# Kernel optimization log

Hardware: AMD Instinct MI355X
Metric: run time of the kernel (lower is better)

The kernel has to match this reference:

```python
import jax, jax.numpy as jnp
import numpy as np

EMBED_DIM = 1024
NUM_HEADS = 16
HEAD_DIM = EMBED_DIM // NUM_HEADS


def setup_inputs() -> dict:
    key = jax.random.key(0)
    ks = jax.random.split(key, 9)
    B, T, D = 2, 4096, EMBED_DIM
    scale = 1.0 / np.sqrt(D)
    x = jax.random.normal(ks[0], (B, T, D), dtype=jnp.float32)
    # nn.Linear weights stored as (out, in); we use (in, out) layout via transpose-free init
    Wq = jax.random.uniform(ks[1], (D, D), dtype=jnp.float32, minval=-scale, maxval=scale)
    Wk = jax.random.uniform(ks[2], (D, D), dtype=jnp.float32, minval=-scale, maxval=scale)
    Wv = jax.random.uniform(ks[3], (D, D), dtype=jnp.float32, minval=-scale, maxval=scale)
    Wo = jax.random.uniform(ks[4], (D, D), dtype=jnp.float32, minval=-scale, maxval=scale)
    bq = jax.random.uniform(ks[5], (D,), dtype=jnp.float32, minval=-scale, maxval=scale)
    bk = jax.random.uniform(ks[6], (D,), dtype=jnp.float32, minval=-scale, maxval=scale)
    bv = jax.random.uniform(ks[7], (D,), dtype=jnp.float32, minval=-scale, maxval=scale)
    bo = jax.random.uniform(ks[8], (D,), dtype=jnp.float32, minval=-scale, maxval=scale)
    return {"x": x, "Wq": Wq, "bq": bq, "Wk": Wk, "bk": bk,
            "Wv": Wv, "bv": bv, "Wo": Wo, "bo": bo}


def reference(x, Wq, bq, Wk, bk, Wv, bv, Wo, bo):
    B, T, D = x.shape
    H, Hd = NUM_HEADS, HEAD_DIM
    q = x @ Wq + bq  # [B,T,D]
    k = x @ Wk + bk
    v = x @ Wv + bv
    # [B,T,D] -> [B,H,T,Hd]
    q = q.reshape(B, T, H, Hd).transpose(0, 2, 1, 3)
    k = k.reshape(B, T, H, Hd).transpose(0, 2, 1, 3)
    v = v.reshape(B, T, H, Hd).transpose(0, 2, 1, 3)
    att = jnp.einsum('bhqd,bhkd->bhqk', q, k) / jnp.sqrt(jnp.float32(Hd))
    causal = jnp.tril(jnp.ones((T, T), dtype=bool))  # True = keep
    att = jnp.where(causal, att, -jnp.inf)
    att = jax.nn.softmax(att, axis=-1)
    out = jnp.einsum('bhqk,bhkd->bhqd', att, v)  # [B,H,T,Hd]
    out = out.transpose(0, 2, 1, 3).reshape(B, T, D)
    return out @ Wo + bo
```

## Files before the change

kernel.cpp:

```cpp
#include <hip/hip_runtime.h>
#include <hip/hip_bf16.h>
#include <math.h>

typedef __bf16 bf16;
typedef __attribute__((ext_vector_type(8))) __bf16 bf16x8;
typedef __attribute__((ext_vector_type(4))) __bf16 bf16x4;
typedef __attribute__((ext_vector_type(4))) short short4v;
typedef __attribute__((ext_vector_type(4))) float f32x4;

#define MFMA16(a,b,c)  __builtin_amdgcn_mfma_f32_16x16x32_bf16((a),(b),(c),0,0,0)
#define MFMAK16(a,b,c) __builtin_amdgcn_mfma_f32_16x16x16bf16_1k((a),(b),(c),0,0,0)

__device__ __forceinline__ void gload16(const void* gp, void* lp) {
  __builtin_amdgcn_global_load_lds(
      (const __attribute__((address_space(1))) void*)gp,
      (__attribute__((address_space(3))) void*)lp, 16, 0, 0);
}

__global__ __launch_bounds__(256) void cast_x(
    const float* __restrict__ x, bf16* __restrict__ xb)
{
  size_t i = ((size_t)blockIdx.x*256 + threadIdx.x) * 8;
  f32x4 a = *(const f32x4*)(x+i);
  f32x4 b = *(const f32x4*)(x+i+4);
  bf16x8 o;
  #pragma unroll
  for (int j=0;j<4;j++) { o[j] = (bf16)a[j]; o[4+j] = (bf16)b[j]; }
  *(bf16x8*)(xb+i) = o;
}

__global__ __launch_bounds__(1024) void tr_cast(
    const float* __restrict__ w0, const float* __restrict__ w1,
    const float* __restrict__ w2, bf16* __restrict__ dst)
{
  __shared__ bf16 tile[64][65];
  const float* src = (blockIdx.z==0)?w0:(blockIdx.z==1)?w1:w2;
  bf16* d = dst + (size_t)blockIdx.z * (1024*1024);
  int x = threadIdx.x, y = threadIdx.y;
  int tc = blockIdx.x, tr = blockIdx.y;
  #pragma unroll
  for (int i=0;i<4;i++) {
    int r = y + i*16;
    tile[r][x] = (bf16)src[(size_t)(tr*64+r)*1024 + tc*64 + x];
  }
  __syncthreads();
  #pragma unroll
  for (int i=0;i<4;i++) {
    int r = y + i*16;
    d[(size_t)(tc*64+r)*1024 + tr*64 + x] = tile[x][r];
  }
}

__global__ __launch_bounds__(1024) void v_tr(
    const bf16* __restrict__ v, bf16* __restrict__ vt)
{
  __shared__ bf16 tile[64][65];
  int x = threadIdx.x, y = threadIdx.y;
  int tt = blockIdx.x;
  int bh = blockIdx.y;
  int b = bh >> 4, h = bh & 15;
  const bf16* src = v + ((size_t)b*4096 + tt*64)*1024 + h*64;
  bf16* dst = vt + ((size_t)bh*64)*4096 + tt*64;
  #pragma unroll
  for (int i=0;i<4;i++) {
    int r = y + i*16;
    tile[r][x] = src[(size_t)r*1024 + x];
  }
  __syncthreads();
  #pragma unroll
  for (int i=0;i<4;i++) {
    int r = y + i*16;
    dst[(size_t)r*4096 + x] = tile[x][r];
  }
}

__global__ __launch_bounds__(256) void gemm_qkv(
    const bf16* __restrict__ A, const bf16* __restrict__ Bt,
    const float* __restrict__ bq, const float* __restrict__ bk, const float* __restrict__ bv,
    bf16* __restrict__ q, bf16* __restrict__ k, bf16* __restrict__ v,
    int M, int K)
{
  __shared__ __align__(16) bf16 As[128*32];
  __shared__ __align__(16) bf16 Bs[128*32];
  const int tid  = threadIdx.x;
  const int wave = tid >> 6;
  const int lane = tid & 63;
  const int l15  = lane & 15;
  const int quad = lane >> 4;
  const int m0 = blockIdx.y * 128;
  const int n0 = blockIdx.x * 128;
  const int wm = (wave >> 1) * 64;
  const int wn = (wave & 1) * 64;
  const int srow = lane >> 2;
  const int scol = (lane & 3) * 8;

  f32x4 acc[4][4];
  #pragma unroll
  for (int i=0;i<4;i++)
    #pragma unroll
    for (int j=0;j<4;j++)
      acc[i][j] = (f32x4){0.f,0.f,0.f,0.f};

  for (int k0 = 0; k0 < K; k0 += 32) {
    __syncthreads();
    #pragma unroll
    for (int p=0;p<2;p++) {
      int c = p*4 + wave;
      int row = c*16 + srow;
      gload16(A  + (size_t)(m0+row)*K + k0 + scol, As + c*512);
      gload16(Bt + (size_t)(n0+row)*K + k0 + scol, Bs + c*512);
    }
    __syncthreads();
    bf16x8 af[4], bfr[4];
    #pragma unroll
    for (int t=0;t<4;t++) {
      af[t]  = *(const bf16x8*)(As + (wm + t*16 + l15)*32 + quad*8);
      bfr[t] = *(const bf16x8*)(Bs + (wn + t*16 + l15)*32 + quad*8);
    }
    #pragma unroll
    for (int mt=0;mt<4;mt++)
      #pragma unroll
      for (int nt=0;nt<4;nt++)
        acc[mt][nt] = MFMA16(af[mt], bfr[nt], acc[mt][nt]);
  }

  const int mat = n0 >> 10;
  const float* bsel = (mat==0) ? bq : (mat==1) ? bk : bv;
  bf16*       osel  = (mat==0) ? q  : (mat==1) ? k  : v;
  const float qsc   = (mat==0) ? 0.1803368801f : 1.0f;
  #pragma unroll
  for (int nt=0;nt<4;nt++) {
    int col = n0 + wn + nt*16 + l15;
    int cw  = col & 1023;
    float bvv = bsel[cw];
    #pragma unroll
    for (int mt=0;mt<4;mt++) {
      int row = m0 + wm + mt*16 + quad*4;
      #pragma unroll
      for (int r=0;r<4;r++)
        osel[(size_t)(row + r)*1024 + cw] = (bf16)((acc[mt][nt][r] + bvv) * qsc);
    }
  }
}

__global__ __launch_bounds__(256) void gemm_out(
    const bf16* __restrict__ A, const bf16* __restrict__ Bt,
    const float* __restrict__ bias, float* __restrict__ C,
    int M, int N, int K)
{
  __shared__ __align__(16) bf16 As[128*32];
  __shared__ __align__(16) bf16 Bs[128*32];
  const int tid  = threadIdx.x;
  const int wave = tid >> 6;
  const int lane = tid & 63;
  const int l15  = lane & 15;
  const int quad = lane >> 4;
  const int m0 = blockIdx.y * 128;
  const int n0 = blockIdx.x * 128;
  const int wm = (wave >> 1) * 64;
  const int wn = (wave & 1) * 64;
  const int srow = lane >> 2;
  const int scol = (lane & 3) * 8;

  f32x4 acc[4][4];
  #pragma unroll
  for (int i=0;i<4;i++)
    #pragma unroll
    for (int j=0;j<4;j++)
      acc[i][j] = (f32x4){0.f,0.f,0.f,0.f};

  for (int k0 = 0; k0 < K; k0 += 32) {
    __syncthreads();
    #pragma unroll
    for (int p=0;p<2;p++) {
      int c = p*4 + wave;
      int row = c*16 + srow;
      gload16(A  + (size_t)(m0+row)*K + k0 + scol, As + c*512);
      gload16(Bt + (size_t)(n0+row)*K + k0 + scol, Bs + c*512);
    }
    __syncthreads();
    bf16x8 af[4], bfr[4];
    #pragma unroll
    for (int t=0;t<4;t++) {
      af[t]  = *(const bf16x8*)(As + (wm + t*16 + l15)*32 + quad*8);
      bfr[t] = *(const bf16x8*)(Bs + (wn + t*16 + l15)*32 + quad*8);
    }
    #pragma unroll
    for (int mt=0;mt<4;mt++)
      #pragma unroll
      for (int nt=0;nt<4;nt++)
        acc[mt][nt] = MFMA16(af[mt], bfr[nt], acc[mt][nt]);
  }

  #pragma unroll
  for (int nt=0;nt<4;nt++) {
    int col = n0 + wn + nt*16 + l15;
    float bvv = bias[col];
    #pragma unroll
    for (int mt=0;mt<4;mt++) {
      int row = m0 + wm + mt*16 + quad*4;
      #pragma unroll
      for (int r=0;r<4;r++)
        C[(size_t)(row + r)*N + col] = acc[mt][nt][r] + bvv;
    }
  }
}

__global__ __launch_bounds__(256, 2) void attn_fwd(
    const bf16* __restrict__ Q, const bf16* __restrict__ Kp,
    const bf16* __restrict__ Vtg, bf16* __restrict__ O)
{
  __shared__ __align__(16) char KsB[2*8192];
  __shared__ __align__(16) char VtB[2*8192];

  const int tid  = threadIdx.x;
  const int w    = tid >> 6;
  const int lane = tid & 63;
  const int l15  = lane & 15;
  const int quad = lane >> 4;

  const int bid = blockIdx.x;
  const int pp  = bid >> 5;
  const int bh  = bid & 31;
  const int h   = bh & 15;
  const int b   = bh >> 4;

  const size_t headoff = (size_t)h * 64;
  const size_t bbase   = (size_t)b * 4096;

  short4v ones_s;
  {
    bf16x4 o1;
    #pragma unroll
    for (int j=0;j<4;j++) o1[j] = (bf16)1.0f;
    ones_s = __builtin_bit_cast(short4v, o1);
  }

  const int kt_row = tid >> 2;
  const int kswz   = (kt_row & 7) << 4;
  const int ks_w0  = kt_row*128 + (((tid & 3)*32)      ^ kswz);
  const int ks_w1  = kt_row*128 + (((tid & 3)*32 + 16) ^ kswz);

  const int vd  = tid >> 2;
  const int vt0 = (tid & 3) * 16;
  int vw[4];
  #pragma unroll
  for (int u=0;u<4;u++)
    vw[u] = vd*128 + (((vt0 + u*4)*2) ^ ((vd & 15) << 3));

  const int s7    = l15 & 7;
  const int ks_r0 = l15*128 + ((quad ^ (s7 & 3)) << 4) + ((s7 >> 2) << 6);
  const int ks_r1 = ks_r0 ^ 64;
  const int vt_rbase = l15*128 + ((quad ^ (l15 & 3)) << 3) + ((l15 >> 2) << 5);
  int vt_r[4];
  #pragma unroll
  for (int tt=0;tt<4;tt++) vt_r[tt] = vt_rbase ^ (tt << 5);

  const bf16* kbase0 = Kp  + (bbase + kt_row)*1024 + headoff + (tid & 3)*16;
  const bf16* vbase0 = Vtg + ((size_t)(bh*64) + vd)*4096 + vt0;

  for (int ph = 0; ph < 2; ++ph) {
    const int qt = ph ? (31 - pp) : pp;
    const int q0 = qt * 128;
    const int ktmax = 2*qt + 1;

    bf16x8 aqA[2], aqB[2];
    {
      int rowA = q0 + w*16 + l15;
      const bf16* qp = Q + (bbase + rowA)*1024 + headoff + quad*8;
      aqA[0] = *(const bf16x8*)(qp);
      aqA[1] = *(const bf16x8*)(qp + 32);
      qp += 64*1024;
      aqB[0] = *(const bf16x8*)(qp);
      aqB[1] = *(const bf16x8*)(qp + 32);
    }

    f32x4 accoA[4], accoB[4], accliA, accliB;
    #pragma unroll
    for (int i=0;i<4;i++) { accoA[i] = (f32x4){0.f,0.f,0.f,0.f}; accoB[i] = (f32x4){0.f,0.f,0.f,0.f}; }
    accliA = (f32x4){0.f,0.f,0.f,0.f};
    accliB = (f32x4){0.f,0.f,0.f,0.f};

    __syncthreads();
    {
      bf16x8 k0 = *(const bf16x8*)(kbase0);
      bf16x8 k1 = *(const bf16x8*)(kbase0 + 8);
      *(bf16x8*)(KsB + ks_w0) = k0;
      *(bf16x8*)(KsB + ks_w1) = k1;
      bf16x8 v0 = *(const bf16x8*)(vbase0);
      bf16x8 v1 = *(const bf16x8*)(vbase0 + 8);
      *(bf16x4*)(VtB + vw[0]) = __builtin_shufflevector(v0, v0, 0,1,2,3);
      *(bf16x4*)(VtB + vw[1]) = __builtin_shufflevector(v0, v0, 4,5,6,7);
      *(bf16x4*)(VtB + vw[2]) = __builtin_shufflevector(v1, v1, 0,1,2,3);
      *(bf16x4*)(VtB + vw[3]) = __builtin_shufflevector(v1, v1, 4,5,6,7);
    }
    __syncthreads();

    const bf16* kpref = kbase0 + 64*1024;
    const bf16* vpref = vbase0 + 64;

    for (int kt = 0; kt <= ktmax; ++kt) {
      const int p = kt & 1;
      const bool pre = (kt < ktmax);

      bf16x8 kr0, kr1, vr0, vr1;
      if (pre) {
        kr0 = *(const bf16x8*)(kpref);
        kr1 = *(const bf16x8*)(kpref + 8);
        vr0 = *(const bf16x8*)(vpref);
        vr1 = *(const bf16x8*)(vpref + 8);
        kpref += 64*1024;
        vpref += 64;
      }

      const char* ksb = KsB + p*8192;
      const char* vtb = VtB + p*8192;

      f32x4 accsA[4], accsB[4];
      #pragma unroll
      for (int i=0;i<4;i++) { accsA[i] = (f32x4){0.f,0.f,0.f,0.f}; accsB[i] = (f32x4){0.f,0.f,0.f,0.f}; }

      __builtin_amdgcn_s_setprio(1);
      #pragma unroll
      for (int kk=0;kk<2;kk++) {
        #pragma unroll
        for (int tt=0;tt<4;tt++) {
          bf16x8 ka = *(const bf16x8*)(ksb + (kk ? ks_r1 : ks_r0) + tt*2048);
          accsA[tt] = MFMA16(ka, aqA[kk], accsA[tt]);
          accsB[tt] = MFMA16(ka, aqB[kk], accsB[tt]);
        }
      }
      __builtin_amdgcn_s_setprio(0);

      short4v ptsA[4], ptsB[4];
      if (kt < 2*qt) {
        #pragma unroll
        for (int tt=0;tt<4;tt++) {
          bf16x4 pa, pb;
          #pragma unroll
          for (int r=0;r<4;r++) {
            pa[r] = (bf16)__builtin_amdgcn_exp2f(fminf(accsA[tt][r], 60.0f));
            pb[r] = (bf16)__builtin_amdgcn_exp2f(fminf(accsB[tt][r], 60.0f));
          }
          ptsA[tt] = __builtin_bit_cast(short4v, pa);
          ptsB[tt] = __builtin_bit_cast(short4v, pb);
        }
      } else {
        const bool adead = (kt > 2*qt);
        #pragma unroll
        for (int tt=0;tt<4;tt++) {
          bf16x4 pa, pb;
          #pragma unroll
          for (int r=0;r<4;r++) {
            const bool tq = (tt*16 + quad*4 + r > w*16 + l15);
            float fa = __builtin_amdgcn_exp2f(fminf(accsA[tt][r], 60.0f));
            if (adead || tq) fa = 0.0f;
            float fb = __builtin_amdgcn_exp2f(fminf(accsB[tt][r], 60.0f));
            if (adead && tq) fb = 0.0f;
            pa[r] = (bf16)fa; pb[r] = (bf16)fb;
          }
          ptsA[tt] = __builtin_bit_cast(short4v, pa);
          ptsB[tt] = __builtin_bit_cast(short4v, pb);
        }
      }

      __builtin_amdgcn_s_setprio(1);
      #pragma unroll
      for (int nt=0;nt<4;nt++) {
        #pragma unroll
        for (int tt=0;tt<4;tt++) {
          bf16x4 va = *(const bf16x4*)(vtb + vt_r[tt] + nt*2048);
          short4v vas = __builtin_bit_cast(short4v, va);
          accoA[nt] = MFMAK16(vas, ptsA[tt], accoA[nt]);
          accoB[nt] = MFMAK16(vas, ptsB[tt], accoB[nt]);
        }
      }
      #pragma unroll
      for (int tt=0;tt<4;tt++) {
        accliA = MFMAK16(ones_s, ptsA[tt], accliA);
        accliB = MFMAK16(ones_s, ptsB[tt], accliB);
      }
      __builtin_amdgcn_s_setprio(0);

      if (pre) {
        char* ksn = KsB + (p^1)*8192;
        char* vtn = VtB + (p^1)*8192;
        *(bf16x8*)(ksn + ks_w0) = kr0;
        *(bf16x8*)(ksn + ks_w1) = kr1;
        *(bf16x4*)(vtn + vw[0]) = __builtin_shufflevector(vr0, vr0, 0,1,2,3);
        *(bf16x4*)(vtn + vw[1]) = __builtin_shufflevector(vr0, vr0, 4,5,6,7);
        *(bf16x4*)(vtn + vw[2]) = __builtin_shufflevector(vr1, vr1, 0,1,2,3);
        *(bf16x4*)(vtn + vw[3]) = __builtin_shufflevector(vr1, vr1, 4,5,6,7);
        __syncthreads();
      }
    }

    {
      float invA = 1.0f / accliA[0];
      float invB = 1.0f / accliB[0];
      int rowA = q0 + w*16 + l15;
      bf16* obA = O + (bbase + rowA)*1024 + headoff;
      bf16* obB = obA + 64*1024;
      #pragma unroll
      for (int nt=0;nt<4;nt++) {
        bf16x4 oA, oB;
        #pragma unroll
        for (int r=0;r<4;r++) {
          oA[r] = (bf16)(accoA[nt][r] * invA);
          oB[r] = (bf16)(accoB[nt][r] * invB);
        }
        *(bf16x4*)(obA + nt*16 + quad*4) = oA;
        *(bf16x4*)(obB + nt*16 + quad*4) = oB;
      }
    }
  }
}

extern "C" void kernel_launch(void* const* d_in, const int* in_sizes, int n_in,
                              void* d_out, int out_size, void* d_ws, size_t ws_size,
                              hipStream_t stream) {
  const float* x  = (const float*)d_in[0];
  const float* Wq = (const float*)d_in[1];
  const float* bq = (const float*)d_in[2];
  const float* Wk = (const float*)d_in[3];
  const float* bk = (const float*)d_in[4];
  const float* Wv = (const float*)d_in[5];
  const float* bv = (const float*)d_in[6];
  const float* Wo = (const float*)d_in[7];
  const float* bo = (const float*)d_in[8];
  float* out = (float*)d_out;

  bf16* ws = (bf16*)d_ws;
  bf16* q  = ws;
  bf16* k  = q + (size_t)8192*1024;
  bf16* v  = k + (size_t)8192*1024;
  bf16* xb = v + (size_t)8192*1024;
  bf16* ao = q;
  bf16* WtQKV = (bf16*)d_out;
  bf16* vT    = (bf16*)d_out;
  bf16* WtO   = xb;

  tr_cast<<<dim3(16,16,3), dim3(64,16), 0, stream>>>(Wq, Wk, Wv, WtQKV);
  cast_x<<<4096, 256, 0, stream>>>(x, xb);
  gemm_qkv<<<dim3(24,64), 256, 0, stream>>>(xb, WtQKV, bq, bk, bv, q, k, v, 8192, 1024);
  v_tr<<<dim3(64,32), dim3(64,16), 0, stream>>>(v, vT);
  tr_cast<<<dim3(16,16,1), dim3(64,16), 0, stream>>>(Wo, Wo, Wo, WtO);
  attn_fwd<<<512, 256, 0, stream>>>(q, k, vT, ao);
  gemm_out<<<dim3(8,64), 256, 0, stream>>>(ao, WtO, bo, out, 8192, 1024, 1024);
}
```

Baseline: 325.5 us.

## Halve attention query tile to 64 rows using 128-thread blocks

Restructures the causal attention kernel so each block handles a 64-row query tile with two waves instead of a 128-row tile with four. Each wave now owns two 16-row groups spaced 16 apart. The grid doubles to 1024 blocks, and the K/V staging is remapped so 128 threads each load half a 64-element row. The aim is finer causal granularity, less masked work on the diagonal tile and more blocks for load balance, at the cost of twice the K/V tile loads per query row and less reuse of each staged tile.

```diff
diff --git a/kernel.cpp b/kernel.cpp
--- a/kernel.cpp
+++ b/kernel.cpp
@@ -206,7 +206,7 @@
   }
 }
 
-__global__ __launch_bounds__(256, 2) void attn_fwd(
+__global__ __launch_bounds__(128, 2) void attn_fwd(
     const bf16* __restrict__ Q, const bf16* __restrict__ Kp,
     const bf16* __restrict__ Vtg, bf16* __restrict__ O)
 {
@@ -236,17 +236,15 @@
     ones_s = __builtin_bit_cast(short4v, o1);
   }
 
-  const int kt_row = tid >> 2;
-  const int kswz   = (kt_row & 7) << 4;
-  const int ks_w0  = kt_row*128 + (((tid & 3)*32)      ^ kswz);
-  const int ks_w1  = kt_row*128 + (((tid & 3)*32 + 16) ^ kswz);
-
-  const int vd  = tid >> 2;
-  const int vt0 = (tid & 3) * 16;
-  int vw[4];
-  #pragma unroll
-  for (int u=0;u<4;u++)
-    vw[u] = vd*128 + (((vt0 + u*4)*2) ^ ((vd & 15) << 3));
+  const int srow  = tid >> 1;
+  const int shalf = tid & 1;
+  int ks_w[4], vw[8];
+  #pragma unroll
+  for (int j=0;j<4;j++)
+    ks_w[j] = srow*128 + (((shalf*64) + 16*j) ^ ((srow & 7) << 4));
+  #pragma unroll
+  for (int c=0;c<8;c++)
+    vw[c] = srow*128 + (((shalf*64) + 8*c) ^ ((srow & 15) << 3));
 
   const int s7    = l15 & 7;
   const int ks_r0 = l15*128 + ((quad ^ (s7 & 3)) << 4) + ((s7 >> 2) << 6);
@@ -256,21 +254,20 @@
   #pragma unroll
   for (int tt=0;tt<4;tt++) vt_r[tt] = vt_rbase ^ (tt << 5);
 
-  const bf16* kbase0 = Kp  + (bbase + kt_row)*1024 + headoff + (tid & 3)*16;
-  const bf16* vbase0 = Vtg + ((size_t)(bh*64) + vd)*4096 + vt0;
+  const bf16* kbase0 = Kp  + (bbase + srow)*1024 + headoff + shalf*32;
+  const bf16* vbase0 = Vtg + ((size_t)(bh*64) + srow)*4096 + shalf*32;
 
   for (int ph = 0; ph < 2; ++ph) {
-    const int qt = ph ? (31 - pp) : pp;
-    const int q0 = qt * 128;
-    const int ktmax = 2*qt + 1;
+    const int qt = ph ? (63 - pp) : pp;
+    const int q0 = qt * 64;
 
     bf16x8 aqA[2], aqB[2];
     {
-      int rowA = q0 + w*16 + l15;
+      int rowA = q0 + 32*w + l15;
       const bf16* qp = Q + (bbase + rowA)*1024 + headoff + quad*8;
       aqA[0] = *(const bf16x8*)(qp);
       aqA[1] = *(const bf16x8*)(qp + 32);
-      qp += 64*1024;
+      qp += 16*1024;
       aqB[0] = *(const bf16x8*)(qp);
       aqB[1] = *(const bf16x8*)(qp + 32);
     }
@@ -283,32 +280,34 @@
 
     __syncthreads();
     {
-      bf16x8 k0 = *(const bf16x8*)(kbase0);
-      bf16x8 k1 = *(const bf16x8*)(kbase0 + 8);
-      *(bf16x8*)(KsB + ks_w0) = k0;
-      *(bf16x8*)(KsB + ks_w1) = k1;
-      bf16x8 v0 = *(const bf16x8*)(vbase0);
-      bf16x8 v1 = *(const bf16x8*)(vbase0 + 8);
-      *(bf16x4*)(VtB + vw[0]) = __builtin_shufflevector(v0, v0, 0,1,2,3);
-      *(bf16x4*)(VtB + vw[1]) = __builtin_shufflevector(v0, v0, 4,5,6,7);
-      *(bf16x4*)(VtB + vw[2]) = __builtin_shufflevector(v1, v1, 0,1,2,3);
-      *(bf16x4*)(VtB + vw[3]) = __builtin_shufflevector(v1, v1, 4,5,6,7);
+      bf16x8 kv[4], vv[4];
+      #pragma unroll
+      for (int j=0;j<4;j++) kv[j] = *(const bf16x8*)(kbase0 + 8*j);
+      #pragma unroll
+      for (int j=0;j<4;j++) vv[j] = *(const bf16x8*)(vbase0 + 8*j);
+      #pragma unroll
+      for (int j=0;j<4;j++) *(bf16x8*)(KsB + ks_w[j]) = kv[j];
+      #pragma unroll
+      for (int j=0;j<4;j++) {
+        *(bf16x4*)(VtB + vw[2*j])   = __builtin_shufflevector(vv[j], vv[j], 0,1,2,3);
+        *(bf16x4*)(VtB + vw[2*j+1]) = __builtin_shufflevector(vv[j], vv[j], 4,5,6,7);
+      }
     }
     __syncthreads();
 
     const bf16* kpref = kbase0 + 64*1024;
     const bf16* vpref = vbase0 + 64;
 
-    for (int kt = 0; kt <= ktmax; ++kt) {
+    for (int kt = 0; kt <= qt; ++kt) {
       const int p = kt & 1;
-      const bool pre = (kt < ktmax);
-
-      bf16x8 kr0, kr1, vr0, vr1;
+      const bool pre = (kt < qt);
+
+      bf16x8 kr[4], vr[4];
       if (pre) {
-        kr0 = *(const bf16x8*)(kpref);
-        kr1 = *(const bf16x8*)(kpref + 8);
-        vr0 = *(const bf16x8*)(vpref);
-        vr1 = *(const bf16x8*)(vpref + 8);
+        #pragma unroll
+        for (int j=0;j<4;j++) kr[j] = *(const bf16x8*)(kpref + 8*j);
+        #pragma unroll
+        for (int j=0;j<4;j++) vr[j] = *(const bf16x8*)(vpref + 8*j);
         kpref += 64*1024;
         vpref += 64;
       }
@@ -333,7 +332,7 @@
       __builtin_amdgcn_s_setprio(0);
 
       short4v ptsA[4], ptsB[4];
-      if (kt < 2*qt) {
+      if (kt < qt) {
         #pragma unroll
         for (int tt=0;tt<4;tt++) {
           bf16x4 pa, pb;
@@ -346,17 +345,17 @@
           ptsB[tt] = __builtin_bit_cast(short4v, pb);
         }
       } else {
-        const bool adead = (kt > 2*qt);
+        const int rowA = 32*w + l15;
         #pragma unroll
         for (int tt=0;tt<4;tt++) {
           bf16x4 pa, pb;
           #pragma unroll
           for (int r=0;r<4;r++) {
-            const bool tq = (tt*16 + quad*4 + r > w*16 + l15);
+            const int tcol = tt*16 + quad*4 + r;
             float fa = __builtin_amdgcn_exp2f(fminf(accsA[tt][r], 60.0f));
-            if (adead || tq) fa = 0.0f;
+            if (tcol > rowA) fa = 0.0f;
             float fb = __builtin_amdgcn_exp2f(fminf(accsB[tt][r], 60.0f));
-            if (adead && tq) fb = 0.0f;
+            if (tcol > rowA + 16) fb = 0.0f;
             pa[r] = (bf16)fa; pb[r] = (bf16)fb;
           }
           ptsA[tt] = __builtin_bit_cast(short4v, pa);
@@ -385,12 +384,13 @@
       if (pre) {
         char* ksn = KsB + (p^1)*8192;
         char* vtn = VtB + (p^1)*8192;
-        *(bf16x8*)(ksn + ks_w0) = kr0;
-        *(bf16x8*)(ksn + ks_w1) = kr1;
-        *(bf16x4*)(vtn + vw[0]) = __builtin_shufflevector(vr0, vr0, 0,1,2,3);
-        *(bf16x4*)(vtn + vw[1]) = __builtin_shufflevector(vr0, vr0, 4,5,6,7);
-        *(bf16x4*)(vtn + vw[2]) = __builtin_shufflevector(vr1, vr1, 0,1,2,3);
-        *(bf16x4*)(vtn + vw[3]) = __builtin_shufflevector(vr1, vr1, 4,5,6,7);
+        #pragma unroll
+        for (int j=0;j<4;j++) *(bf16x8*)(ksn + ks_w[j]) = kr[j];
+        #pragma unroll
+        for (int j=0;j<4;j++) {
+          *(bf16x4*)(vtn + vw[2*j])   = __builtin_shufflevector(vr[j], vr[j], 0,1,2,3);
+          *(bf16x4*)(vtn + vw[2*j+1]) = __builtin_shufflevector(vr[j], vr[j], 4,5,6,7);
+        }
         __syncthreads();
       }
     }
@@ -398,9 +398,9 @@
     {
       float invA = 1.0f / accliA[0];
       float invB = 1.0f / accliB[0];
-      int rowA = q0 + w*16 + l15;
+      int rowA = q0 + 32*w + l15;
       bf16* obA = O + (bbase + rowA)*1024 + headoff;
-      bf16* obB = obA + 64*1024;
+      bf16* obB = obA + 16*1024;
       #pragma unroll
       for (int nt=0;nt<4;nt++) {
         bf16x4 oA, oB;
@@ -445,6 +445,6 @@
   gemm_qkv<<<dim3(24,64), 256, 0, stream>>>(xb, WtQKV, bq, bk, bv, q, k, v, 8192, 1024);
   v_tr<<<dim3(64,32), dim3(64,16), 0, stream>>>(v, vT);
   tr_cast<<<dim3(16,16,1), dim3(64,16), 0, stream>>>(Wo, Wo, Wo, WtO);
-  attn_fwd<<<512, 256, 0, stream>>>(q, k, vT, ao);
+  attn_fwd<<<1024, 128, 0, stream>>>(q, k, vT, ao);
   gemm_out<<<dim3(8,64), 256, 0, stream>>>(ao, WtO, bo, out, 8192, 1024, 1024);
 }
```

New measurement: 327.4 us. About the same (+0.6%).
